# Kernel optimization log

Hardware: AMD Instinct MI355X
Metric: run time of the kernel (lower is better)

The kernel has to match this reference:

```python
import jax, jax.numpy as jnp
import numpy as np

NH, DK, DV, D = 8, 64, 64, 768
DECAY = 0.95
WRITE_STRENGTH = 0.1


def setup_inputs() -> dict:
    key = jax.random.key(0)
    ks = jax.random.split(key, 6)
    s = 0.02  # small init scale for projection weights
    return {
        "x": jax.random.normal(ks[0], (4, 4096, D), dtype=jnp.float32),
        "w_key": jax.random.normal(ks[1], (NH * DK, D), dtype=jnp.float32) * s,
        "w_value": jax.random.normal(ks[2], (NH * DV, D), dtype=jnp.float32) * s,
        "w_query": jax.random.normal(ks[3], (NH * DK, D), dtype=jnp.float32) * s,
        "w_gate": jax.random.normal(ks[4], (NH, D), dtype=jnp.float32) * s,
        "w_out": jax.random.normal(ks[5], (D, NH * DV), dtype=jnp.float32) * s,
    }


def reference(x, w_key, w_value, w_query, w_gate, w_out):
    B, S, _ = x.shape
    # Batched projections (torch Linear: y = x @ W.T)
    k = (x @ w_key.T).reshape(B, S, NH, DK)
    v = (x @ w_value.T).reshape(B, S, NH, DV)
    q = (x @ w_query.T).reshape(B, S, NH, DK)
    gate = jax.nn.sigmoid(x @ w_gate.T)  # (B, S, NH)

    # Writes only use batch element 0 (mirrors k[0], v[0], gate[0] in source)
    k0 = k[0]      # (S, NH, DK)
    v0 = v[0]      # (S, NH, DV)
    g0 = gate[0]   # (S, NH)

    def step(fw, inp):
        q_t, k0_t, v0_t, g0_t = inp
        # Read BEFORE this step's decay+write
        retrieved = jnp.einsum('bhk,hkv->bhv', q_t, fw)  # (B, NH, DV)
        write = (WRITE_STRENGTH * g0_t)[:, None, None] * (k0_t[:, :, None] * v0_t[:, None, :])
        fw_new = DECAY * fw + jax.lax.stop_gradient(write)
        return fw_new, retrieved

    fw0 = jnp.zeros((NH, DK, DV), dtype=x.dtype)
    inputs = (q.transpose(1, 0, 2, 3), k0, v0, g0)  # time-major
    _, retrieved = jax.lax.scan(step, fw0, inputs)   # (S, B, NH, DV)
    retrieved = retrieved.transpose(1, 0, 2, 3).reshape(B, S, NH * DV)
    return x + retrieved @ w_out.T
```

## Files before the change

kernel.cpp:

```cpp
#include <hip/hip_runtime.h>
#include <hip/hip_bf16.h>

typedef __hip_bfloat16 bf16;
typedef __attribute__((ext_vector_type(8))) short   bf16x8;
typedef __attribute__((ext_vector_type(4))) float   f32x4;

#define B_   4
#define S_   4096
#define D_   768
#define NH_  8
#define DK_  64
#define DV_  64
#define CH_  64
#define NCH_ (S_/CH_)
#define DECAY_ 0.95f
#define WSTR_  0.1f

__device__ __forceinline__ float b2f(bf16 v) { return __bfloat162float(v); }
__device__ __forceinline__ bf16  f2b(float v) { return __float2bfloat16(v); }

__device__ __forceinline__ void gl2lds16(const bf16* g, bf16* lds) {
    __builtin_amdgcn_global_load_lds(
        (const __attribute__((address_space(1))) void*)g,
        (__attribute__((address_space(3))) void*)lds, 16, 0, 0);
}

__global__ __launch_bounds__(192) void cast_fused(const float* __restrict__ x,
                                                  bf16* __restrict__ xb,
                                                  const float* __restrict__ wg,
                                                  float* __restrict__ wgt,
                                                  const float* __restrict__ wq,
                                                  const float* __restrict__ wk,
                                                  const float* __restrict__ wv,
                                                  const float* __restrict__ wo,
                                                  bf16* __restrict__ dq, bf16* __restrict__ dk,
                                                  bf16* __restrict__ dv, bf16* __restrict__ dob) {
    const int tid = threadIdx.x;
    if (blockIdx.x >= (B_ * S_)) {
        const int idx = blockIdx.x - B_ * S_;
        const int which = idx >> 9, b = idx & 511;
        const float* src = which == 0 ? wq : which == 1 ? wk : which == 2 ? wv : wo;
        bf16*       dst = which == 0 ? dq : which == 1 ? dk : which == 2 ? dv : dob;
        const int i = (b * 192 + tid) * 4;
        const float4 v = *reinterpret_cast<const float4*>(src + i);
        union { bf16 b4[4]; ushort4 u; } t;
        t.b4[0] = f2b(v.x); t.b4[1] = f2b(v.y); t.b4[2] = f2b(v.z); t.b4[3] = f2b(v.w);
        *reinterpret_cast<ushort4*>(dst + i) = t.u;
        return;
    }
    const int s = blockIdx.x;
    const float4 v = *reinterpret_cast<const float4*>(x + (size_t)s * D_ + tid * 4);
    union { bf16 b4[4]; ushort4 u; } t;
    t.b4[0] = f2b(v.x); t.b4[1] = f2b(v.y); t.b4[2] = f2b(v.z); t.b4[3] = f2b(v.w);
    *reinterpret_cast<ushort4*>(xb + (size_t)s * D_ + tid * 4) = t.u;

    if (s < S_) {
        __shared__ float red[3 * 8];
        float p[8];
        const float* wgp = wg + tid * 4;
        #pragma unroll
        for (int h = 0; h < 8; h++) {
            const float4 wv4 = *reinterpret_cast<const float4*>(wgp + h * D_);
            p[h] = v.x * wv4.x + v.y * wv4.y + v.z * wv4.z + v.w * wv4.w;
        }
        #pragma unroll
        for (int h = 0; h < 8; h++)
            #pragma unroll
            for (int off = 32; off; off >>= 1) p[h] += __shfl_down(p[h], off);
        const int w = tid >> 6, lane = tid & 63;
        if (lane == 0) {
            #pragma unroll
            for (int h = 0; h < 8; h++) red[w * 8 + h] = p[h];
        }
        __syncthreads();
        if (tid < 8) {
            const float sum = red[tid] + red[8 + tid] + red[16 + tid];
            wgt[s * NH_ + tid] = WSTR_ / (1.f + expf(-sum));
        }
    }
}

template<typename TC, int ADDX, int NITER>
__device__ __forceinline__ void gemm_body(bf16* As, bf16* Bs,
                                          const bf16* __restrict__ A,
                                          const bf16* __restrict__ Bm,
                                          const float* __restrict__ X,
                                          TC* __restrict__ C,
                                          int bm, int bn, int K, int N) {
    const int tid = threadIdx.x, lane = tid & 63, w = tid >> 6;
    const int quad = lane >> 4, l16 = lane & 15;
    const int wm = (w >> 1) * 64, wn = (w & 1) * 64;
    const int lrow = lane >> 3;
    const int lcol = ((lane & 7) ^ lrow) * 8;

    f32x4 acc[4][4] = {};
    bf16x8 brg[4];

    auto STAGE_A = [&](int it, int buf) {
        const int k0 = it * 64;
        bf16* Ad = As + buf * 8192;
        #pragma unroll
        for (int c = 0; c < 4; c++) {
            const int seg = w * 4 + c;
            const int row = seg * 8 + lrow;
            gl2lds16(A + (size_t)(bm + row) * K + k0 + lcol, &Ad[seg * 512]);
        }
    };
    auto BLOAD = [&](int it) {
        const int k0 = it * 64;
        #pragma unroll
        for (int c = 0; c < 4; c++) {
            const int row = (w * 4 + c) * 8 + lrow;
            brg[c] = *reinterpret_cast<const bf16x8*>(
                Bm + (size_t)(bn + row) * K + k0 + lcol);
        }
    };
    auto WRITE_B = [&]() {
        #pragma unroll
        for (int c = 0; c < 4; c++) {
            const int seg = w * 4 + c;
            *reinterpret_cast<bf16x8*>(&Bs[seg * 512 + lane * 8]) = brg[c];
        }
    };

    BLOAD(0);
    STAGE_A(0, 0);
    asm volatile("s_waitcnt vmcnt(4)" ::: "memory");
    WRITE_B();

    for (int it = 0; it < NITER; ++it) {
        const int cur = it & 1;
        if (it + 1 < NITER) {
            BLOAD(it + 1);
            STAGE_A(it + 1, cur ^ 1);
            asm volatile("s_waitcnt vmcnt(8)" ::: "memory");
        } else {
            asm volatile("s_waitcnt vmcnt(0)" ::: "memory");
        }
        asm volatile("s_waitcnt lgkmcnt(0)" ::: "memory");
        __builtin_amdgcn_s_barrier();
        asm volatile("" ::: "memory");

        const bf16* Ar = As + cur * 8192;
        #pragma unroll
        for (int kh = 0; kh < 2; kh++) {
            bf16x8 af[4], bfr[4];
            #pragma unroll
            for (int t = 0; t < 4; t++) {
                const int cb = ((kh * 4 + quad) ^ (l16 & 7)) * 8;
                af[t]  = *reinterpret_cast<const bf16x8*>(&Ar[(wm + t * 16 + l16) * 64 + cb]);
                bfr[t] = *reinterpret_cast<const bf16x8*>(&Bs[(wn + t * 16 + l16) * 64 + cb]);
            }
            #pragma unroll
            for (int mt = 0; mt < 4; mt++)
                #pragma unroll
                for (int nt = 0; nt < 4; nt++)
                    acc[mt][nt] = __builtin_amdgcn_mfma_f32_16x16x32_bf16(
                        af[mt], bfr[nt], acc[mt][nt], 0, 0, 0);
        }
        if (it + 1 < NITER) {
            asm volatile("" ::: "memory");
            __builtin_amdgcn_s_barrier();
            asm volatile("s_waitcnt vmcnt(4)" ::: "memory");
            WRITE_B();
            asm volatile("" ::: "memory");
        }
    }

    #pragma unroll
    for (int mt = 0; mt < 4; mt++)
        #pragma unroll
        for (int nt = 0; nt < 4; nt++)
            #pragma unroll
            for (int r = 0; r < 4; r++) {
                const int m = bm + wm + mt * 16 + quad * 4 + r;
                const int n = bn + wn + nt * 16 + l16;
                float v = acc[mt][nt][r];
                if (ADDX) v += X[(size_t)m * N + n];
                if (sizeof(TC) == 2) *(bf16*)&C[(size_t)m * N + n] = f2b(v);
                else                 *(float*)&C[(size_t)m * N + n] = v;
            }
}

__global__ __launch_bounds__(256) void proj_fused(const bf16* __restrict__ xb,
                                                  const bf16* __restrict__ wqb,
                                                  const bf16* __restrict__ wkb,
                                                  const bf16* __restrict__ wvb,
                                                  bf16* __restrict__ qbuf,
                                                  bf16* __restrict__ k0buf,
                                                  bf16* __restrict__ v0buf) {
    __shared__ bf16 As[2 * 128 * 64];
    __shared__ bf16 Bs[128 * 64];
    const int id = blockIdx.x;
    const int xcd = id & 7;
    int j = id >> 3;
    const bf16* Bm; bf16* C; int bm, bn;
    if (j < 64) {
        bm = (xcd + ((j >> 2) << 3)) * 128;
        bn = (j & 3) * 128;
        Bm = wqb; C = qbuf;
    } else {
        j -= 64;
        bm = (xcd + ((j >> 3) << 3)) * 128;
        const int b8 = j & 7;
        bn = (b8 & 3) * 128;
        Bm = (b8 < 4) ? wkb : wvb;
        C  = (b8 < 4) ? k0buf : v0buf;
    }
    gemm_body<bf16, 0, 12>(As, Bs, xb, Bm, nullptr, C, bm, bn, D_, 512);
}

__global__ __launch_bounds__(256) void gemm_out(const bf16* __restrict__ retr,
                                                const bf16* __restrict__ wob,
                                                const float* __restrict__ x,
                                                float* __restrict__ out) {
    __shared__ bf16 As[2 * 128 * 64];
    __shared__ bf16 Bs[128 * 64];
    const int gx = gridDim.x, gy = gridDim.y;
    const int L = blockIdx.y * gx + blockIdx.x;
    const int rpx = gy >> 3;
    const int xcd = L & 7;
    const int i   = L >> 3;
    const int by = xcd * rpx + i / gx;
    const int bx = i % gx;
    gemm_body<float, 1, 8>(As, Bs, retr, wob, x, out, by * 128, bx * 128, 512, D_);
}

__global__ __launch_bounds__(256) void chunk_sums(const bf16* __restrict__ k0,
                                                  const bf16* __restrict__ v0,
                                                  const float* __restrict__ wgt,
                                                  bf16* __restrict__ lsumsT) {
    const int n = blockIdx.x, h = blockIdx.y;
    __shared__ float ks[CH_][65];
    __shared__ float vs[CH_][64];
    __shared__ float cw[CH_];
    const int tid = threadIdx.x;
    for (int e = tid; e < CH_ * 64; e += 256) {
        const int r = e >> 6, c = e & 63;
        const int t = n * CH_ + r;
        ks[r][c] = b2f(k0[(size_t)t * (NH_ * DK_) + h * DK_ + c]);
        vs[r][c] = b2f(v0[(size_t)t * (NH_ * DV_) + h * DV_ + c]);
    }
    if (tid < CH_) {
        const int t = n * CH_ + tid;
        cw[tid] = powf(DECAY_, (float)(CH_ - 1 - tid)) * wgt[t * NH_ + h];
    }
    __syncthreads();
    const int j = tid & 63, ig = tid >> 6;
    float acc[16] = {};
    for (int idx = 0; idx < CH_; idx++) {
        const float ck = cw[idx] * ks[idx][j];
        #pragma unroll
        for (int r = 0; r < 16; r++) acc[r] += vs[idx][ig * 16 + r] * ck;
    }
    bf16* outp = lsumsT + ((size_t)(n * NH_ + h)) * (DK_ * DV_);
    #pragma unroll
    for (int r = 0; r < 16; r++) outp[(ig * 16 + r) * 64 + j] = f2b(acc[r]);
}

__device__ __forceinline__ void cvt4(ushort4 u, float f[4]) {
    union { unsigned u; float f; } c;
    c.u = (unsigned)u.x << 16; f[0] = c.f;
    c.u = (unsigned)u.y << 16; f[1] = c.f;
    c.u = (unsigned)u.z << 16; f[2] = c.f;
    c.u = (unsigned)u.w << 16; f[3] = c.f;
}

__global__ __launch_bounds__(256) void chunk_output(const bf16* __restrict__ q,
                                                    const bf16* __restrict__ k0,
                                                    const bf16* __restrict__ v0,
                                                    const float* __restrict__ wgt,
                                                    const bf16* __restrict__ lsumsT,
                                                    bf16* __restrict__ retr) {
    const int n = blockIdx.x, h = blockIdx.y;
    __shared__ bf16 QsAm[4][64 * 64];
    __shared__ bf16 Ks[64 * 64];
    __shared__ bf16 FWT[64 * 64];
    __shared__ bf16 VT[64 * 72];
    __shared__ float dpow[64], winv[64];
    const int tid = threadIdx.x, lane = tid & 63, w = tid >> 6;
    const int quad = lane >> 4, l16 = lane & 15;
    const int t0 = n * CH_;
    const int lrow = lane >> 3;
    const int lcol = ((lane & 7) ^ lrow) * 8;

    #pragma unroll
    for (int seg = 0; seg < 8; seg++) {
        const int row = seg * 8 + lrow;
        gl2lds16(q + ((size_t)(w * S_ + t0 + row)) * 512 + h * 64 + lcol, &QsAm[w][seg * 512]);
    }
    #pragma unroll
    for (int c = 0; c < 2; c++) {
        const int seg = w * 2 + c;
        const int row = seg * 8 + lrow;
        gl2lds16(k0 + ((size_t)(t0 + row)) * 512 + h * 64 + lcol, &Ks[seg * 512]);
    }

    {
        float fwacc[16] = {};
        const float dcp[4] = { 1.0f, 0.0375241f, 1.40806e-3f, 5.28365e-5f };
        #pragma unroll
        for (int jj = 1; jj <= 4; jj++) {
            const int nm = n - jj;
            if (nm < 0) break;
            const ushort* Lp = (const ushort*)(lsumsT + ((size_t)(nm * NH_ + h)) * 4096) + tid * 16;
            #pragma unroll
            for (int u = 0; u < 4; u++) {
                float f[4];
                cvt4(reinterpret_cast<const ushort4*>(Lp)[u], f);
                #pragma unroll
                for (int e = 0; e < 4; e++) fwacc[u * 4 + e] += dcp[jj - 1] * f[e];
            }
        }
        const int frow = tid >> 2;
        #pragma unroll
        for (int half = 0; half < 2; half++) {
            const int cb = (tid & 3) * 2 + half;
            union { bf16 b8v[8]; bf16x8 v; } t;
            #pragma unroll
            for (int e = 0; e < 8; e++) t.b8v[e] = f2b(fwacc[half * 8 + e]);
            *reinterpret_cast<bf16x8*>(&FWT[frow * 64 + (cb ^ (frow & 7)) * 8]) = t.v;
        }
    }
    {
        ushort4 vreg[4];
        const int jb = (tid & 15) * 4;
        const int sb = tid >> 4;
        #pragma unroll
        for (int it = 0; it < 4; it++)
            vreg[it] = *reinterpret_cast<const ushort4*>(
                v0 + ((size_t)(t0 + sb + it * 16)) * 512 + h * 64 + jb);
        ushort* VTu = reinterpret_cast<ushort*>(VT);
        #pragma unroll
        for (int it = 0; it < 4; it++) {
            const int s = sb + it * 16;
            VTu[(jb + 0) * 72 + s] = vreg[it].x;
            VTu[(jb + 1) * 72 + s] = vreg[it].y;
            VTu[(jb + 2) * 72 + s] = vreg[it].z;
            VTu[(jb + 3) * 72 + s] = vreg[it].w;
        }
    }
    if (tid < 64) {
        dpow[tid] = powf(DECAY_, (float)tid);
        winv[tid] = wgt[(t0 + tid) * NH_ + h] * powf(DECAY_, -(float)(tid + 1));
    }
    __syncthreads();

    const int cb0 = ((quad) ^ (l16 & 7)) * 8;
    const int cb1 = ((4 + quad) ^ (l16 & 7)) * 8;
    bf16* Qw = &QsAm[w][0];

    bf16x8 af[4][2];
    #pragma unroll
    for (int mt = 0; mt < 4; mt++) {
        af[mt][0] = *reinterpret_cast<const bf16x8*>(&Qw[(mt * 16 + l16) * 64 + cb0]);
        af[mt][1] = *reinterpret_cast<const bf16x8*>(&Qw[(mt * 16 + l16) * 64 + cb1]);
    }

    f32x4 acc[4][4] = {};
    #pragma unroll
    for (int kh = 0; kh < 2; kh++) {
        bf16x8 bk[4];
        #pragma unroll
        for (int nt = 0; nt < 4; nt++)
            bk[nt] = *reinterpret_cast<const bf16x8*>(
                &Ks[(nt * 16 + l16) * 64 + (kh ? cb1 : cb0)]);
        #pragma unroll
        for (int mt = 0; mt < 4; mt++)
            #pragma unroll
            for (int nt = 0; nt < 4; nt++)
                acc[mt][nt] = __builtin_amdgcn_mfma_f32_16x16x32_bf16(
                    af[mt][kh], bk[nt], acc[mt][nt], 0, 0, 0);
    }

    const float pmt[4] = { 1.0f, 0.4401266694f, 0.1937114891f, 0.0852578070f };
    const f32x4 dpb = *reinterpret_cast<const f32x4*>(&dpow[quad * 4]);
    float winv_l[4];
    #pragma unroll
    for (int nt = 0; nt < 4; nt++) winv_l[nt] = winv[nt * 16 + l16];
    #pragma unroll
    for (int mt = 0; mt < 4; mt++)
        #pragma unroll
        for (int nt = 0; nt < 4; nt++)
            #pragma unroll
            for (int r = 0; r < 4; r++) {
                const int tt = mt * 16 + quad * 4 + r;
                const int s = nt * 16 + l16;
                const float v = (s < tt) ? acc[mt][nt][r] * (dpb[r] * pmt[mt]) * winv_l[nt] : 0.f;
                Qw[tt * 64 + (((s >> 3) ^ (tt & 7)) << 3) + (s & 7)] = f2b(v);
            }

    f32x4 o[4][4] = {};
    #pragma unroll
    for (int kh = 0; kh < 2; kh++) {
        bf16x8 ff[4];
        #pragma unroll
        for (int nt = 0; nt < 4; nt++)
            ff[nt] = *reinterpret_cast<const bf16x8*>(
                &FWT[(nt * 16 + l16) * 64 + (kh ? cb1 : cb0)]);
        #pragma unroll
        for (int mt = 0; mt < 4; mt++)
            #pragma unroll
            for (int nt = 0; nt < 4; nt++)
                o[mt][nt] = __builtin_amdgcn_mfma_f32_16x16x32_bf16(
                    af[mt][kh], ff[nt], o[mt][nt], 0, 0, 0);
    }
    #pragma unroll
    for (int mt = 0; mt < 4; mt++)
        #pragma unroll
        for (int nt = 0; nt < 4; nt++)
            #pragma unroll
            for (int r = 0; r < 4; r++) o[mt][nt][r] *= dpb[r] * pmt[mt];

    #pragma unroll
    for (int kh = 0; kh < 2; kh++) {
        bf16x8 am[4], vf[4];
        #pragma unroll
        for (int mt = 0; mt < 4; mt++)
            am[mt] = *reinterpret_cast<const bf16x8*>(
                &Qw[(mt * 16 + l16) * 64 + (kh ? cb1 : cb0)]);
        #pragma unroll
        for (int nt = 0; nt < 4; nt++)
            vf[nt] = *reinterpret_cast<const bf16x8*>(
                &VT[(nt * 16 + l16) * 72 + kh * 32 + quad * 8]);
        #pragma unroll
        for (int mt = 0; mt < 4; mt++)
            #pragma unroll
            for (int nt = 0; nt < 4; nt++)
                o[mt][nt] = __builtin_amdgcn_mfma_f32_16x16x32_bf16(
                    am[mt], vf[nt], o[mt][nt], 0, 0, 0);
    }

    #pragma unroll
    for (int mt = 0; mt < 4; mt++)
        #pragma unroll
        for (int nt = 0; nt < 4; nt++)
            #pragma unroll
            for (int r = 0; r < 4; r++) {
                const int tt = mt * 16 + quad * 4 + r;
                retr[((size_t)(w * S_ + t0 + tt)) * 512 + h * 64 + nt * 16 + l16] =
                    f2b(o[mt][nt][r]);
            }
}

extern "C" void kernel_launch(void* const* d_in, const int* in_sizes, int n_in,
                              void* d_out, int out_size, void* d_ws, size_t ws_size,
                              hipStream_t stream) {
    const float* x  = (const float*)d_in[0];
    const float* wk = (const float*)d_in[1];
    const float* wv = (const float*)d_in[2];
    const float* wq = (const float*)d_in[3];
    const float* wg = (const float*)d_in[4];
    const float* wo = (const float*)d_in[5];
    float* out = (float*)d_out;

    const size_t MB1 = 1ull << 20;
    char* w = (char*)d_ws;
    bf16*  qbuf    = (bf16*)(w);
    bf16*  k0buf   = (bf16*)(w + 16 * MB1);
    bf16*  v0buf   = (bf16*)(w + 20 * MB1);
    float* wgt     = (float*)(w + 24 * MB1);
    bf16*  wqb     = (bf16*)(w + 24 * MB1 + (128ull<<10));
    bf16*  wkb     = (bf16*)(w + 24 * MB1 + (128ull<<10) + 1*786432);
    bf16*  wvb     = (bf16*)(w + 24 * MB1 + (128ull<<10) + 2*786432);
    bf16*  wob     = (bf16*)(w + 24 * MB1 + (128ull<<10) + 3*786432);
    bf16*  lsumsT  = (bf16*)(w + 28 * MB1);
    bf16*  retr    = (bf16*)(w + 32 * MB1);
    bf16*  xb      = (bf16*)(w + 48 * MB1);

    const int MB = B_ * S_;

    cast_fused<<<MB + 2048, 192, 0, stream>>>(x, xb, wg, wgt,
                                              wq, wk, wv, wo, wqb, wkb, wvb, wob);

    proj_fused<<<768, 256, 0, stream>>>(xb, wqb, wkb, wvb, qbuf, k0buf, v0buf);

    chunk_sums<<<dim3(NCH_, NH_), 256, 0, stream>>>(k0buf, v0buf, wgt, lsumsT);
    chunk_output<<<dim3(NCH_, NH_), 256, 0, stream>>>(qbuf, k0buf, v0buf, wgt, lsumsT, retr);

    gemm_out<<<dim3(D_ / 128, MB / 128), 256, 0, stream>>>(retr, wob, x, out);
}
```

Before: 212.2 us.

## Stage B tile via direct global-to-LDS loads and hoist fragment reads before MFMA

The B operand is now loaded straight into LDS with global_load_lds, replacing the register round-trip and ds_write. All A/B fragments for both k-halves are read into registers before the barrier. The next B tile is then issued so its load overlaps the MFMA work. Launch bounds add a minimum-occupancy hint of 3 blocks per CU. This cuts VGPR traffic and one barrier per iteration, but B stays single-buffered, so correctness depends on the barrier ordering, and the occupancy hint may cause register spills.

```diff
diff --git a/kernel.cpp b/kernel.cpp
--- a/kernel.cpp
+++ b/kernel.cpp
@@ -94,7 +94,6 @@
     const int lcol = ((lane & 7) ^ lrow) * 8;
 
     f32x4 acc[4][4] = {};
-    bf16x8 brg[4];
 
     auto STAGE_A = [&](int it, int buf) {
         const int k0 = it * 64;
@@ -106,65 +105,52 @@
             gl2lds16(A + (size_t)(bm + row) * K + k0 + lcol, &Ad[seg * 512]);
         }
     };
-    auto BLOAD = [&](int it) {
+    auto STAGE_B = [&](int it) {
         const int k0 = it * 64;
-        #pragma unroll
-        for (int c = 0; c < 4; c++) {
-            const int row = (w * 4 + c) * 8 + lrow;
-            brg[c] = *reinterpret_cast<const bf16x8*>(
-                Bm + (size_t)(bn + row) * K + k0 + lcol);
-        }
-    };
-    auto WRITE_B = [&]() {
         #pragma unroll
         for (int c = 0; c < 4; c++) {
             const int seg = w * 4 + c;
-            *reinterpret_cast<bf16x8*>(&Bs[seg * 512 + lane * 8]) = brg[c];
+            const int row = seg * 8 + lrow;
+            gl2lds16(Bm + (size_t)(bn + row) * K + k0 + lcol, &Bs[seg * 512]);
         }
     };
 
-    BLOAD(0);
     STAGE_A(0, 0);
-    asm volatile("s_waitcnt vmcnt(4)" ::: "memory");
-    WRITE_B();
+    STAGE_B(0);
 
     for (int it = 0; it < NITER; ++it) {
         const int cur = it & 1;
         if (it + 1 < NITER) {
-            BLOAD(it + 1);
             STAGE_A(it + 1, cur ^ 1);
-            asm volatile("s_waitcnt vmcnt(8)" ::: "memory");
+            asm volatile("s_waitcnt vmcnt(4)" ::: "memory");
         } else {
             asm volatile("s_waitcnt vmcnt(0)" ::: "memory");
         }
+        __builtin_amdgcn_s_barrier();
+        asm volatile("" ::: "memory");
+
+        const bf16* Ar = As + cur * 8192;
+        bf16x8 af[2][4], bfr[2][4];
+        #pragma unroll
+        for (int kh = 0; kh < 2; kh++)
+            #pragma unroll
+            for (int t = 0; t < 4; t++) {
+                const int cb = ((kh * 4 + quad) ^ (l16 & 7)) * 8;
+                af[kh][t]  = *reinterpret_cast<const bf16x8*>(&Ar[(wm + t * 16 + l16) * 64 + cb]);
+                bfr[kh][t] = *reinterpret_cast<const bf16x8*>(&Bs[(wn + t * 16 + l16) * 64 + cb]);
+            }
         asm volatile("s_waitcnt lgkmcnt(0)" ::: "memory");
         __builtin_amdgcn_s_barrier();
-        asm volatile("" ::: "memory");
-
-        const bf16* Ar = As + cur * 8192;
-        #pragma unroll
-        for (int kh = 0; kh < 2; kh++) {
-            bf16x8 af[4], bfr[4];
-            #pragma unroll
-            for (int t = 0; t < 4; t++) {
-                const int cb = ((kh * 4 + quad) ^ (l16 & 7)) * 8;
-                af[t]  = *reinterpret_cast<const bf16x8*>(&Ar[(wm + t * 16 + l16) * 64 + cb]);
-                bfr[t] = *reinterpret_cast<const bf16x8*>(&Bs[(wn + t * 16 + l16) * 64 + cb]);
-            }
+        if (it + 1 < NITER) STAGE_B(it + 1);
+
+        #pragma unroll
+        for (int kh = 0; kh < 2; kh++)
             #pragma unroll
             for (int mt = 0; mt < 4; mt++)
                 #pragma unroll
                 for (int nt = 0; nt < 4; nt++)
                     acc[mt][nt] = __builtin_amdgcn_mfma_f32_16x16x32_bf16(
-                        af[mt], bfr[nt], acc[mt][nt], 0, 0, 0);
-        }
-        if (it + 1 < NITER) {
-            asm volatile("" ::: "memory");
-            __builtin_amdgcn_s_barrier();
-            asm volatile("s_waitcnt vmcnt(4)" ::: "memory");
-            WRITE_B();
-            asm volatile("" ::: "memory");
-        }
+                        af[kh][mt], bfr[kh][nt], acc[mt][nt], 0, 0, 0);
     }
 
     #pragma unroll
@@ -182,7 +168,7 @@
             }
 }
 
-__global__ __launch_bounds__(256) void proj_fused(const bf16* __restrict__ xb,
+__global__ __launch_bounds__(256, 3) void proj_fused(const bf16* __restrict__ xb,
                                                   const bf16* __restrict__ wqb,
                                                   const bf16* __restrict__ wkb,
                                                   const bf16* __restrict__ wvb,
@@ -210,7 +196,7 @@
     gemm_body<bf16, 0, 12>(As, Bs, xb, Bm, nullptr, C, bm, bn, D_, 512);
 }
 
-__global__ __launch_bounds__(256) void gemm_out(const bf16* __restrict__ retr,
+__global__ __launch_bounds__(256, 3) void gemm_out(const bf16* __restrict__ retr,
                                                 const bf16* __restrict__ wob,
                                                 const float* __restrict__ x,
                                                 float* __restrict__ out) {
```

New measurement: 185.5 us. 12.6% less time.
